# Kernel tuning notes

Hardware: AMD Instinct MI355X
Metric: run time of the kernel (lower is better)

The kernel has to match this reference:

```python
import jax, jax.numpy as jnp
import numpy as np

INPUT_DIM = 1024
HIDDEN_DIM = 1024


def setup_inputs() -> dict:
    key = jax.random.key(0)
    ks = jax.random.split(key, 7)
    B, S = 4, 2048
    s = 1.0 / np.sqrt(INPUT_DIM)
    x = jax.random.normal(ks[0], (B, S, INPUT_DIM), dtype=jnp.float32)
    Wq = jax.random.normal(ks[1], (HIDDEN_DIM, INPUT_DIM), dtype=jnp.float32) * s
    bq = jnp.zeros((HIDDEN_DIM,), dtype=jnp.float32)
    Wk = jax.random.normal(ks[2], (HIDDEN_DIM, INPUT_DIM), dtype=jnp.float32) * s
    bk = jnp.zeros((HIDDEN_DIM,), dtype=jnp.float32)
    Wv = jax.random.normal(ks[3], (HIDDEN_DIM, INPUT_DIM), dtype=jnp.float32) * s
    bv = jnp.zeros((HIDDEN_DIM,), dtype=jnp.float32)
    return {"x": x, "Wq": Wq, "bq": bq, "Wk": Wk, "bk": bk, "Wv": Wv, "bv": bv}


def reference(x, Wq, bq, Wk, bk, Wv, bv):
    # Linear layers: y = x @ W.T + b (torch nn.Linear convention)
    q = jnp.einsum('bsi,hi->bsh', x, Wq) + bq
    k = jnp.einsum('bsi,hi->bsh', x, Wk) + bk
    v = jnp.einsum('bsi,hi->bsh', x, Wv) + bv
    scale = 1.0 / jnp.sqrt(jnp.asarray(q.shape[-1], dtype=q.dtype))
    scores = jnp.einsum('bsh,bth->bst', q, k) * scale  # [B,S,S]
    attention_weights = jax.nn.softmax(scores, axis=-1)
    weighted_sum = jnp.einsum('bst,bth->bsh', attention_weights, v)
    return (weighted_sum, attention_weights)
```

## Files before the change

kernel.cpp:

```cpp
#include <hip/hip_runtime.h>
#include <hip/hip_bf16.h>
#include <cstdint>


typedef __bf16 bf16x8 __attribute__((ext_vector_type(8)));
typedef float  f32x4  __attribute__((ext_vector_type(4)));

__device__ __forceinline__ void load_lds16(const __bf16* g, __bf16* l) {
    __builtin_amdgcn_global_load_lds(
        (const __attribute__((address_space(1))) void*)g,
        (__attribute__((address_space(3))) void*)l,
        16, 0, 0);
}

__global__ __launch_bounds__(256) void cvt_all(
        const float* __restrict__ x,
        const float* __restrict__ wq, const float* __restrict__ wk,
        const float* __restrict__ wv,
        const float* __restrict__ bq, const float* __restrict__ bk,
        const float* __restrict__ bv,
        __bf16* __restrict__ xb, __bf16* __restrict__ wb,
        float* __restrict__ bias3) {
    const long NX = 1048576, NW = 131072;
    long i = (long)blockIdx.x * 256 + threadIdx.x;
    const float* src; __bf16* dst; long c;
    if (i < NX) { src = x; dst = xb; c = i; }
    else if (i < NX + 3 * NW) {
        long j = i - NX;
        src = (j < NW) ? wq : (j < 2 * NW) ? wk : wv;
        c = j % NW;
        dst = wb + (j / NW) * (NW * 8);
    } else if (i < NX + 3 * NW + 384) {
        long cidx = i - (NX + 3 * NW);
        int seg = (int)(cidx >> 7);
        const float* bs = (seg == 0) ? bq : (seg == 1) ? bk : bv;
        long off = (cidx & 127) * 8;
        float4 a = *(const float4*)(bs + off);
        float4 b = *(const float4*)(bs + off + 4);
        *(float4*)(bias3 + cidx * 8)     = a;
        *(float4*)(bias3 + cidx * 8 + 4) = b;
        return;
    } else return;
    const float4* s4 = (const float4*)src;
    float4 a = s4[2 * c], b = s4[2 * c + 1];
    bf16x8 o;
    o[0] = (__bf16)a.x; o[1] = (__bf16)a.y; o[2] = (__bf16)a.z; o[3] = (__bf16)a.w;
    o[4] = (__bf16)b.x; o[5] = (__bf16)b.y; o[6] = (__bf16)b.z; o[7] = (__bf16)b.w;
    ((bf16x8*)dst)[c] = o;
}

template <int MODE>
__global__ __launch_bounds__(256, 4) void gemm_nt(
        const __bf16* __restrict__ A, const __bf16* __restrict__ Bt,
        void* __restrict__ C0, void* __restrict__ C1, void* __restrict__ C2,
        const float* __restrict__ bias,
        int lda, int ldb, int ldc, long sA, long sB, long sC,
        int K, float scale) {
    __shared__ __bf16 smem[16384];
    __bf16* lA = smem;
    __bf16* lB = smem + 8192;

    const int tid  = threadIdx.x;
    const int lane = tid & 63;
    const int wave = tid >> 6;
    const int mblk = blockIdx.y * 128;
    const int nblk = blockIdx.x * 128;
    const int z    = blockIdx.z;
    A  += (long)z * sA;
    Bt += (long)z * sB;

    const int wm = (wave >> 1) * 64;
    const int wn = (wave & 1) * 64;

    f32x4 zero = {0.f, 0.f, 0.f, 0.f};
    f32x4 acc[4][4];
#pragma unroll
    for (int i = 0; i < 4; ++i)
#pragma unroll
        for (int j = 0; j < 4; ++j) acc[i][j] = zero;

    const int rsel = lane & 15;
    const int quad = lane >> 4;

    int srow[4], scol[4];
#pragma unroll
    for (int it = 0; it < 4; ++it) {
        int s  = tid + it * 256;
        srow[it] = s >> 3;
        scol[it] = ((s & 7) ^ (srow[it] & 7)) * 8;
    }

    for (int k0 = 0; k0 < K; k0 += 64) {
#pragma unroll
        for (int it = 0; it < 4; ++it) {
            int s = tid + it * 256;
            load_lds16(A  + (long)(mblk + srow[it]) * lda + k0 + scol[it], lA + s * 8);
            load_lds16(Bt + (long)(nblk + srow[it]) * ldb + k0 + scol[it], lB + s * 8);
        }
        __syncthreads();

#pragma unroll
        for (int half = 0; half < 2; ++half) {
            const int cq = quad + half * 4;
            bf16x8 fa[4], fb[4];
#pragma unroll
            for (int i = 0; i < 4; ++i) {
                int ra = wm + i * 16 + rsel;
                fa[i] = *(const bf16x8*)&lA[(ra * 8 + (cq ^ (ra & 7))) * 8];
                int rb = wn + i * 16 + rsel;
                fb[i] = *(const bf16x8*)&lB[(rb * 8 + (cq ^ (rb & 7))) * 8];
            }
#pragma unroll
            for (int i = 0; i < 4; ++i)
#pragma unroll
                for (int j = 0; j < 4; ++j)
                    acc[i][j] = __builtin_amdgcn_mfma_f32_16x16x32_bf16(
                        fa[i], fb[j], acc[i][j], 0, 0, 0);
        }
        __syncthreads();
    }

    const int rq = quad * 4;
    if constexpr (MODE == 0) {
        if (nblk >= 2048) {
            __bf16* tbuf = smem;
#pragma unroll
            for (int i = 0; i < 4; ++i) {
#pragma unroll
                for (int j = 0; j < 4; ++j) {
                    const int n_loc = wn + j * 16 + rsel;
                    const float bv = bias[nblk + n_loc];
                    const int m_loc = wm + i * 16 + rq;
                    const int c  = m_loc >> 3;
                    const int cs = c ^ (n_loc & 15);
                    __bf16* dst = &tbuf[n_loc * 128 + cs * 8 + (m_loc & 7)];
                    __bf16 tmp[4];
#pragma unroll
                    for (int r = 0; r < 4; ++r) tmp[r] = (__bf16)(acc[i][j][r] + bv);
                    *(uint64_t*)dst = *(const uint64_t*)tmp;
                }
            }
            __syncthreads();
            {
                __bf16* vt = (__bf16*)C2;
                const int n_loc = tid & 127;
                const int cpart = tid >> 7;
                const long b = mblk >> 11;
                const long t0 = mblk & 2047;
                const long h  = nblk - 2048 + n_loc;
                __bf16* gdst = vt + b * (1024L * 2048) + h * 2048 + t0;
#pragma unroll
                for (int s = 0; s < 8; ++s) {
                    int c  = cpart * 8 + s;
                    int cs = c ^ (n_loc & 15);
                    bf16x8 vchunk = *(const bf16x8*)&tbuf[n_loc * 128 + cs * 8];
                    *(bf16x8*)(gdst + c * 8) = vchunk;
                }
            }
        } else {
#pragma unroll
            for (int i = 0; i < 4; ++i) {
#pragma unroll
                for (int j = 0; j < 4; ++j) {
                    const int n = nblk + wn + j * 16 + rsel;
                    __bf16* C = (n < 1024) ? (__bf16*)C0 : (__bf16*)C1;
                    const int col = n & 1023;
                    float bv = bias[n];
#pragma unroll
                    for (int r = 0; r < 4; ++r) {
                        int m = mblk + wm + i * 16 + rq + r;
                        C[(long)m * ldc + col] = (__bf16)(acc[i][j][r] + bv);
                    }
                }
            }
        }
    } else if constexpr (MODE == 1) {
        __bf16* C = (__bf16*)C0 + (long)z * sC;
#pragma unroll
        for (int i = 0; i < 4; ++i) {
#pragma unroll
            for (int j = 0; j < 4; ++j) {
                const int n = nblk + wn + j * 16 + rsel;
#pragma unroll
                for (int r = 0; r < 4; ++r) {
                    int m = mblk + wm + i * 16 + rq + r;
                    C[(long)m * ldc + n] = (__bf16)(acc[i][j][r] * scale);
                }
            }
        }
    } else {
        float* C = (float*)C0 + (long)z * sC;
#pragma unroll
        for (int i = 0; i < 4; ++i) {
#pragma unroll
            for (int j = 0; j < 4; ++j) {
                const int n = nblk + wn + j * 16 + rsel;
#pragma unroll
                for (int r = 0; r < 4; ++r) {
                    int m = mblk + wm + i * 16 + rq + r;
                    C[(long)m * ldc + n] = acc[i][j][r];
                }
            }
        }
    }
}

__global__ __launch_bounds__(256) void softmax_rows(
        __bf16* __restrict__ Pb, float* __restrict__ P) {
    const long row = blockIdx.x;
    __bf16* pb = Pb + row * 2048;
    float*  p  = P  + row * 2048;
    const int tid  = threadIdx.x;
    const int lane = tid & 63;
    const int wave = tid >> 6;

    bf16x8 v = ((const bf16x8*)pb)[tid];
    float e[8];
#pragma unroll
    for (int i = 0; i < 8; ++i) e[i] = (float)v[i];

    float mx = e[0];
#pragma unroll
    for (int i = 1; i < 8; ++i) mx = fmaxf(mx, e[i]);
#pragma unroll
    for (int o = 1; o < 64; o <<= 1) mx = fmaxf(mx, __shfl_xor(mx, o, 64));

    __shared__ float redm[4], reds[4];
    if (lane == 0) redm[wave] = mx;
    __syncthreads();
    mx = fmaxf(fmaxf(redm[0], redm[1]), fmaxf(redm[2], redm[3]));

    float sum = 0.f;
#pragma unroll
    for (int i = 0; i < 8; ++i) { e[i] = __expf(e[i] - mx); sum += e[i]; }
#pragma unroll
    for (int o = 1; o < 64; o <<= 1) sum += __shfl_xor(sum, o, 64);
    if (lane == 0) reds[wave] = sum;
    __syncthreads();
    sum = reds[0] + reds[1] + reds[2] + reds[3];
    const float inv = 1.f / sum;

    float4 o0, o1;
    o0.x = e[0] * inv; o0.y = e[1] * inv; o0.z = e[2] * inv; o0.w = e[3] * inv;
    o1.x = e[4] * inv; o1.y = e[5] * inv; o1.z = e[6] * inv; o1.w = e[7] * inv;
    ((float4*)p)[tid * 2]     = o0;
    ((float4*)p)[tid * 2 + 1] = o1;
    bf16x8 ob;
    ob[0] = (__bf16)o0.x; ob[1] = (__bf16)o0.y; ob[2] = (__bf16)o0.z; ob[3] = (__bf16)o0.w;
    ob[4] = (__bf16)o1.x; ob[5] = (__bf16)o1.y; ob[6] = (__bf16)o1.z; ob[7] = (__bf16)o1.w;
    ((bf16x8*)pb)[tid] = ob;
}

extern "C" void kernel_launch(void* const* d_in, const int* in_sizes, int n_in,
                              void* d_out, int out_size, void* d_ws, size_t ws_size,
                              hipStream_t stream) {
    const float* x  = (const float*)d_in[0];
    const float* Wq = (const float*)d_in[1];
    const float* bq = (const float*)d_in[2];
    const float* Wk = (const float*)d_in[3];
    const float* bk = (const float*)d_in[4];
    const float* Wv = (const float*)d_in[5];
    const float* bv = (const float*)d_in[6];

    const int  S = 2048, H = 1024, I = 1024, B = 4;
    const long MS = (long)B * S;
    float* out_ws  = (float*)d_out;
    float* out_att = (float*)d_out + (long)B * S * H;

    char* w = (char*)d_ws;
    __bf16* x_bf   = (__bf16*)w; w += MS * I * 2;
    __bf16* wqkv   = (__bf16*)w; w += (long)3 * H * I * 2;
    float*  bias3  = (float*)w;  w += 4096 * 4;
    __bf16* q_bf   = (__bf16*)w; w += MS * H * 2;
    __bf16* k_bf   = (__bf16*)w; w += MS * H * 2;
    __bf16* vt_bf  = (__bf16*)w; w += MS * H * 2;
    __bf16* p_bf   = (__bf16*)w; w += (long)B * S * S * 2;

    {
        long tot = 1048576 + 3 * 131072 + 384;
        cvt_all<<<dim3((unsigned)((tot + 255) / 256)), dim3(256), 0, stream>>>(
            x, Wq, Wk, Wv, bq, bk, bv, x_bf, wqkv, bias3);
    }

    gemm_nt<0><<<dim3(24, 64, 1), dim3(256), 0, stream>>>(
        x_bf, wqkv, q_bf, k_bf, vt_bf, bias3,
        1024, 1024, 1024, 0, 0, 0, 1024, 1.f);

    gemm_nt<1><<<dim3(16, 16, 4), dim3(256), 0, stream>>>(
        q_bf, k_bf, p_bf, nullptr, nullptr, nullptr,
        1024, 1024, 2048, (long)S * H, (long)S * H, (long)S * S, 1024, 0.03125f);

    softmax_rows<<<dim3(8192), dim3(256), 0, stream>>>(p_bf, out_att);

    gemm_nt<2><<<dim3(8, 16, 4), dim3(256), 0, stream>>>(
        p_bf, vt_bf, out_ws, nullptr, nullptr, nullptr,
        2048, 2048, 1024, (long)S * S, (long)S * H, (long)S * H, 2048, 1.f);
}
```

Before: 296.6 us.

## Fuse softmax into QK and PV GEMMs via unnormalized exp and row sums

Drops the standalone softmax kernel. The QK GEMM epilogue now writes exp(score) without subtracting the row max and stores partial row sums per 64-column block. The PV GEMM reduces those partials into per-row inverse sums, scales its output by them, and has one N-block per K-step write the normalized attention weights in fp32 from the LDS tile. This removes a full read/write pass over the score matrix, but skipping the max subtraction risks overflow for large scores and adds uncoalesced-ish extra stores inside the GEMM main loop.

Measured after the change: 291.6 us. Within noise of the previous version (-1.7%).

```diff
diff --git a/kernel.cpp b/kernel.cpp
--- a/kernel.cpp
+++ b/kernel.cpp
@@ -57,6 +57,7 @@
         int lda, int ldb, int ldc, long sA, long sB, long sC,
         int K, float scale) {
     __shared__ __bf16 smem[16384];
+    __shared__ float linv[128];
     __bf16* lA = smem;
     __bf16* lB = smem + 8192;
 
@@ -90,6 +91,16 @@
         scol[it] = ((s & 7) ^ (srow[it] & 7)) * 8;
     }
 
+    if constexpr (MODE == 2) {
+        if (tid < 128) {
+            const float* ps = (const float*)C1 + (long)z * 65536 + (mblk + tid);
+            float ssum = 0.f;
+#pragma unroll
+            for (int nb = 0; nb < 32; ++nb) ssum += ps[nb * 2048];
+            linv[tid] = 1.f / ssum;
+        }
+    }
+
     for (int k0 = 0; k0 < K; k0 += 64) {
 #pragma unroll
         for (int it = 0; it < 4; ++it) {
@@ -116,6 +127,26 @@
                 for (int j = 0; j < 4; ++j)
                     acc[i][j] = __builtin_amdgcn_mfma_f32_16x16x32_bf16(
                         fa[i], fb[j], acc[i][j], 0, 0, 0);
+        }
+
+        if constexpr (MODE == 2) {
+            if (((k0 >> 6) & 7) == (int)blockIdx.x) {
+                float* wout = (float*)C2 + (long)z * (2048L * 2048);
+#pragma unroll
+                for (int it = 0; it < 4; ++it) {
+                    int s = tid + it * 256;
+                    bf16x8 ch = *(const bf16x8*)&lA[s * 8];
+                    float iv = linv[srow[it]];
+                    float4 w0, w1;
+                    w0.x = (float)ch[0] * iv; w0.y = (float)ch[1] * iv;
+                    w0.z = (float)ch[2] * iv; w0.w = (float)ch[3] * iv;
+                    w1.x = (float)ch[4] * iv; w1.y = (float)ch[5] * iv;
+                    w1.z = (float)ch[6] * iv; w1.w = (float)ch[7] * iv;
+                    float* wp = wout + (long)(mblk + srow[it]) * 2048 + k0 + scol[it];
+                    *(float4*)wp       = w0;
+                    *(float4*)(wp + 4) = w1;
+                }
+            }
         }
         __syncthreads();
     }
@@ -176,6 +207,12 @@
         }
     } else if constexpr (MODE == 1) {
         __bf16* C = (__bf16*)C0 + (long)z * sC;
+        float* psum = (float*)C1 + (long)z * 65536;
+        float vsum[4][4];
+#pragma unroll
+        for (int i = 0; i < 4; ++i)
+#pragma unroll
+            for (int r = 0; r < 4; ++r) vsum[i][r] = 0.f;
 #pragma unroll
         for (int i = 0; i < 4; ++i) {
 #pragma unroll
@@ -184,12 +221,29 @@
 #pragma unroll
                 for (int r = 0; r < 4; ++r) {
                     int m = mblk + wm + i * 16 + rq + r;
-                    C[(long)m * ldc + n] = (__bf16)(acc[i][j][r] * scale);
-                }
-            }
+                    float e = __expf(acc[i][j][r] * scale);
+                    C[(long)m * ldc + n] = (__bf16)e;
+                    vsum[i][r] += e;
+                }
+            }
+        }
+#pragma unroll
+        for (int o = 1; o < 16; o <<= 1)
+#pragma unroll
+            for (int i = 0; i < 4; ++i)
+#pragma unroll
+                for (int r = 0; r < 4; ++r)
+                    vsum[i][r] += __shfl_xor(vsum[i][r], o, 64);
+        if (rsel == 0) {
+            const int nb2 = (nblk + wn) >> 6;
+#pragma unroll
+            for (int i = 0; i < 4; ++i)
+#pragma unroll
+                for (int r = 0; r < 4; ++r)
+                    psum[nb2 * 2048 + mblk + wm + i * 16 + rq + r] = vsum[i][r];
         }
     } else {
-        float* C = (float*)C0 + (long)z * sC;
+        float* Cz = (float*)C0 + (long)z * sC;
 #pragma unroll
         for (int i = 0; i < 4; ++i) {
 #pragma unroll
@@ -198,57 +252,11 @@
 #pragma unroll
                 for (int r = 0; r < 4; ++r) {
                     int m = mblk + wm + i * 16 + rq + r;
-                    C[(long)m * ldc + n] = acc[i][j][r];
-                }
-            }
-        }
-    }
-}
-
-__global__ __launch_bounds__(256) void softmax_rows(
-        __bf16* __restrict__ Pb, float* __restrict__ P) {
-    const long row = blockIdx.x;
-    __bf16* pb = Pb + row * 2048;
-    float*  p  = P  + row * 2048;
-    const int tid  = threadIdx.x;
-    const int lane = tid & 63;
-    const int wave = tid >> 6;
-
-    bf16x8 v = ((const bf16x8*)pb)[tid];
-    float e[8];
-#pragma unroll
-    for (int i = 0; i < 8; ++i) e[i] = (float)v[i];
-
-    float mx = e[0];
-#pragma unroll
-    for (int i = 1; i < 8; ++i) mx = fmaxf(mx, e[i]);
-#pragma unroll
-    for (int o = 1; o < 64; o <<= 1) mx = fmaxf(mx, __shfl_xor(mx, o, 64));
-
-    __shared__ float redm[4], reds[4];
-    if (lane == 0) redm[wave] = mx;
-    __syncthreads();
-    mx = fmaxf(fmaxf(redm[0], redm[1]), fmaxf(redm[2], redm[3]));
-
-    float sum = 0.f;
-#pragma unroll
-    for (int i = 0; i < 8; ++i) { e[i] = __expf(e[i] - mx); sum += e[i]; }
-#pragma unroll
-    for (int o = 1; o < 64; o <<= 1) sum += __shfl_xor(sum, o, 64);
-    if (lane == 0) reds[wave] = sum;
-    __syncthreads();
-    sum = reds[0] + reds[1] + reds[2] + reds[3];
-    const float inv = 1.f / sum;
-
-    float4 o0, o1;
-    o0.x = e[0] * inv; o0.y = e[1] * inv; o0.z = e[2] * inv; o0.w = e[3] * inv;
-    o1.x = e[4] * inv; o1.y = e[5] * inv; o1.z = e[6] * inv; o1.w = e[7] * inv;
-    ((float4*)p)[tid * 2]     = o0;
-    ((float4*)p)[tid * 2 + 1] = o1;
-    bf16x8 ob;
-    ob[0] = (__bf16)o0.x; ob[1] = (__bf16)o0.y; ob[2] = (__bf16)o0.z; ob[3] = (__bf16)o0.w;
-    ob[4] = (__bf16)o1.x; ob[5] = (__bf16)o1.y; ob[6] = (__bf16)o1.z; ob[7] = (__bf16)o1.w;
-    ((bf16x8*)pb)[tid] = ob;
+                    Cz[(long)m * ldc + n] = acc[i][j][r] * linv[wm + i * 16 + rq + r];
+                }
+            }
+        }
+    }
 }
 
 extern "C" void kernel_launch(void* const* d_in, const int* in_sizes, int n_in,
@@ -275,6 +283,7 @@
     __bf16* k_bf   = (__bf16*)w; w += MS * H * 2;
     __bf16* vt_bf  = (__bf16*)w; w += MS * H * 2;
     __bf16* p_bf   = (__bf16*)w; w += (long)B * S * S * 2;
+    float* psum = (float*)x_bf;
 
     {
         long tot = 1048576 + 3 * 131072 + 384;
@@ -287,12 +296,10 @@
         1024, 1024, 1024, 0, 0, 0, 1024, 1.f);
 
     gemm_nt<1><<<dim3(16, 16, 4), dim3(256), 0, stream>>>(
-        q_bf, k_bf, p_bf, nullptr, nullptr, nullptr,
+        q_bf, k_bf, p_bf, psum, nullptr, nullptr,
         1024, 1024, 2048, (long)S * H, (long)S * H, (long)S * S, 1024, 0.03125f);
 
-    softmax_rows<<<dim3(8192), dim3(256), 0, stream>>>(p_bf, out_att);
-
     gemm_nt<2><<<dim3(8, 16, 4), dim3(256), 0, stream>>>(
-        p_bf, vt_bf, out_ws, nullptr, nullptr, nullptr,
+        p_bf, vt_bf, out_ws, psum, out_att, nullptr,
         2048, 2048, 1024, (long)S * S, (long)S * H, (long)S * H, 2048, 1.f);
 }
```
